# Performance work log

Measured on AMD Instinct MI355X. Metric: run time of the kernel, lower is better.

Reference implementation:

```python
import jax, jax.numpy as jnp
import numpy as np

B, N, DIN, DOUT = 16, 256, 64, 64
TEMP = 2.0          # temperatures[0]
POOL_K = 0.5        # pool_ratios[0]
BN_EPS = 1e-5


def setup_inputs() -> dict:
    key = jax.random.key(0)
    ks = jax.random.split(key, 8)
    g = lambda i, shape: (jax.random.normal(ks[i], shape, jnp.float32) * 0.08)
    return {
        "x": jax.random.normal(ks[0], (B, N, DIN), jnp.float32),
        # GraphAttentionLayer params
        "W_att": g(1, (DIN, DOUT)), "b_att": jnp.zeros((DOUT,), jnp.float32),
        "att_w": g(2, (DOUT,)),                      # att_weight [DOUT,1] squeezed
        "W_pwa": g(3, (DIN, DOUT)), "b_pwa": jnp.zeros((DOUT,), jnp.float32),
        "W_pna": g(4, (DIN, DOUT)), "b_pna": jnp.zeros((DOUT,), jnp.float32),
        "bn_scale": jnp.ones((DOUT,), jnp.float32),
        "bn_bias": jnp.zeros((DOUT,), jnp.float32),
        # GraphPool params
        "pool_w": g(5, (DOUT,)), "pool_b": jnp.zeros((), jnp.float32),
    }


def reference(x, W_att, b_att, att_w, W_pwa, b_pwa, W_pna, b_pna,
              bn_scale, bn_bias, pool_w, pool_b):
    # --- GraphAttentionLayer (eval mode: dropout = identity) ---
    # pairwise node multiplication: [B, i, j, DIN]
    pm = x[:, :, None, :] * x[:, None, :, :]
    att = jnp.tanh(jnp.einsum('bijd,de->bije', pm, W_att) + b_att)   # [B,N,N,DOUT]
    logits = jnp.einsum('bije,e->bij', att, att_w) / TEMP            # [B,N,N]
    # torch softmax over dim=-2 of [B,i,j,1] == axis j (the aggregated axis)
    A = jax.nn.softmax(logits, axis=2)                               # [B,N,N]
    agg = jnp.einsum('bij,bjd->bid', A, x)                           # [B,N,DIN]
    h = (agg @ W_pwa + b_pwa) + (x @ W_pna + b_pna)                  # [B,N,DOUT]
    # BatchNorm1d eval with running_mean=0, running_var=1
    h = h * (bn_scale / jnp.sqrt(1.0 + BN_EPS)) + bn_bias
    h = jax.nn.selu(h)
    # --- GraphPool (eval mode: dropout = identity) ---
    scores = jax.nn.sigmoid(h @ pool_w + pool_b)                     # [B,N]
    k = max(int(N * POOL_K), 1)
    _, idx = jax.lax.top_k(scores, k)                                # [B,k]
    hw = h * scores[:, :, None]
    out = jnp.take_along_axis(hw, idx[:, :, None], axis=1)           # [B,k,DOUT]
    return out
```

## Files before the change

kernel.cpp:

```cpp
#include <hip/hip_runtime.h>
#include <hip/hip_bf16.h>
#include <math.h>

#define BB 16
#define NN 256
#define DD 64
#define KTOP 128

typedef short s16x8 __attribute__((ext_vector_type(8)));
typedef float f32x4 __attribute__((ext_vector_type(4)));

typedef union { s16x8 v; unsigned u[4]; } frag_u;
typedef union { __hip_bfloat162 b2; unsigned u; } cvu;

__device__ __forceinline__ float asf(unsigned u){ union{unsigned u;float f;}c; c.u=u; return c.f; }

__device__ __forceinline__ void split2(float v0, float v1, unsigned& hu, unsigned& lu) {
    cvu c; c.b2 = __float22bfloat162_rn(make_float2(v0, v1));
    unsigned h = c.u;
    float l0 = v0 - asf(h << 16);
    float l1 = v1 - asf(h & 0xffff0000u);
    c.b2 = __float22bfloat162_rn(make_float2(l0, l1));
    hu = h; lu = c.u;
}

__global__ __launch_bounds__(512, 4) void k_fused(
    const float* __restrict__ x, const float* __restrict__ W_att,
    const float* __restrict__ b_att, const float* __restrict__ att_w,
    const float* __restrict__ Wpwa, const float* __restrict__ bpwa,
    const float* __restrict__ Wpna, const float* __restrict__ bpna,
    const float* __restrict__ bnsc, const float* __restrict__ bnbi,
    const float* __restrict__ poolw, const float* __restrict__ poolb,
    float* __restrict__ hbuf, float* __restrict__ scores)
{
    const int ig = blockIdx.x;
    const int b  = blockIdx.y;
    const int tid = threadIdx.x;
    const int w = tid >> 6, lane = tid & 63;
    const int quad = lane >> 4, c16 = lane & 15;
    const int jb = w * 32;
    const int ibase = ig * 4;

    __shared__ s16x8 sB[2][2][4][2][64];
    __shared__ float sXi[4 * 64];
    __shared__ float sL[4][256];
    __shared__ float sAgg[4][64];

    if (tid < 256) sXi[tid] = x[(b * NN + ibase + (tid >> 6)) * DD + (tid & 63)];

    const float L2E2 = 2.8853900817779268f;
    float bawL[4], aww[4];
    #pragma unroll
    for (int et = 0; et < 4; ++et) {
        bawL[et] = b_att[et * 16 + c16] * L2E2;
        aww[et]  = att_w[et * 16 + c16];
    }
    float halfS;
    {
        float sa = aww[0] + aww[1] + aww[2] + aww[3];
        sa += __shfl_xor(sa, 1); sa += __shfl_xor(sa, 2);
        sa += __shfl_xor(sa, 4); sa += __shfl_xor(sa, 8);
        halfS = 0.5f * sa;
    }

    const int bks = w >> 2, bet = w & 3;
    float wv[8];
    {
        const float* wp = &W_att[(bks * 32 + quad * 8) * 64 + bet * 16 + c16];
        #pragma unroll
        for (int t = 0; t < 8; ++t) wv[t] = wp[t * 64];
    }

    frag_u Ah[2][2], Al[2][2];
    #pragma unroll
    for (int jt = 0; jt < 2; ++jt) {
        #pragma unroll
        for (int ks = 0; ks < 2; ++ks) {
            const float* xr = &x[(b * NN + jb + jt * 16 + c16) * DD + ks * 32 + quad * 8];
            float4 a0 = *(const float4*)xr;
            float4 a1 = *(const float4*)(xr + 4);
            split2(a0.x, a0.y, Ah[jt][ks].u[0], Al[jt][ks].u[0]);
            split2(a0.z, a0.w, Ah[jt][ks].u[1], Al[jt][ks].u[1]);
            split2(a1.x, a1.y, Ah[jt][ks].u[2], Al[jt][ks].u[2]);
            split2(a1.z, a1.w, Ah[jt][ks].u[3], Al[jt][ks].u[3]);
        }
    }
    __syncthreads();

    {
        const float* xr = &sXi[0 * 64 + bks * 32 + quad * 8];
        float4 c0 = *(const float4*)xr;
        float4 c1 = *(const float4*)(xr + 4);
        float xiv[8] = {c0.x,c0.y,c0.z,c0.w,c1.x,c1.y,c1.z,c1.w};
        frag_u bh, bl;
        split2(wv[0] * xiv[0], wv[1] * xiv[1], bh.u[0], bl.u[0]);
        split2(wv[2] * xiv[2], wv[3] * xiv[3], bh.u[1], bl.u[1]);
        split2(wv[4] * xiv[4], wv[5] * xiv[5], bh.u[2], bl.u[2]);
        split2(wv[6] * xiv[6], wv[7] * xiv[7], bh.u[3], bl.u[3]);
        sB[0][bks][bet][0][lane] = bh.v;
        sB[0][bks][bet][1][lane] = bl.v;
    }

    #pragma unroll
    for (int ii = 0; ii < 4; ++ii) {
        __syncthreads();

        if (ii < 3) {
            const float* xr = &sXi[(ii + 1) * 64 + bks * 32 + quad * 8];
            float4 c0 = *(const float4*)xr;
            float4 c1 = *(const float4*)(xr + 4);
            float xiv[8] = {c0.x,c0.y,c0.z,c0.w,c1.x,c1.y,c1.z,c1.w};
            frag_u bh, bl;
            split2(wv[0] * xiv[0], wv[1] * xiv[1], bh.u[0], bl.u[0]);
            split2(wv[2] * xiv[2], wv[3] * xiv[3], bh.u[1], bl.u[1]);
            split2(wv[4] * xiv[4], wv[5] * xiv[5], bh.u[2], bl.u[2]);
            split2(wv[6] * xiv[6], wv[7] * xiv[7], bh.u[3], bl.u[3]);
            sB[(ii + 1) & 1][bks][bet][0][lane] = bh.v;
            sB[(ii + 1) & 1][bks][bet][1][lane] = bl.v;
        }

        const int cur = ii & 1;
        float p[2][4];
        #pragma unroll
        for (int jt = 0; jt < 2; ++jt)
            #pragma unroll
            for (int r = 0; r < 4; ++r) p[jt][r] = 0.0f;

        #pragma unroll
        for (int eth = 0; eth < 2; ++eth) {
            f32x4 acc[2][2];
            #pragma unroll
            for (int jt = 0; jt < 2; ++jt)
                #pragma unroll
                for (int e2 = 0; e2 < 2; ++e2)
                    acc[jt][e2] = (f32x4){0.f, 0.f, 0.f, 0.f};

            #pragma unroll
            for (int ks = 0; ks < 2; ++ks) {
                #pragma unroll
                for (int e2 = 0; e2 < 2; ++e2) {
                    const int et = eth * 2 + e2;
                    s16x8 bh = sB[cur][ks][et][0][lane];
                    s16x8 bl = sB[cur][ks][et][1][lane];
                    #pragma unroll
                    for (int jt = 0; jt < 2; ++jt) {
                        acc[jt][e2] = __builtin_amdgcn_mfma_f32_16x16x32_bf16(Ah[jt][ks].v, bh, acc[jt][e2], 0, 0, 0);
                        acc[jt][e2] = __builtin_amdgcn_mfma_f32_16x16x32_bf16(Al[jt][ks].v, bh, acc[jt][e2], 0, 0, 0);
                        acc[jt][e2] = __builtin_amdgcn_mfma_f32_16x16x32_bf16(Ah[jt][ks].v, bl, acc[jt][e2], 0, 0, 0);
                    }
                }
            }

            #pragma unroll
            for (int e2 = 0; e2 < 2; ++e2) {
                const int et = eth * 2 + e2;
                #pragma unroll
                for (int jt = 0; jt < 2; ++jt) {
                    #pragma unroll
                    for (int r = 0; r < 4; ++r) {
                        float arg = fmaf(acc[jt][e2][r], L2E2, bawL[et]);
                        float m = __builtin_amdgcn_exp2f(arg);
                        float rc = __builtin_amdgcn_rcpf(m + 1.0f);
                        p[jt][r] = fmaf(aww[et], rc, p[jt][r]);
                    }
                }
            }
        }

        #pragma unroll
        for (int jt = 0; jt < 2; ++jt) {
            #pragma unroll
            for (int r = 0; r < 4; ++r) {
                float s = p[jt][r];
                s += __shfl_xor(s, 1);
                s += __shfl_xor(s, 2);
                s += __shfl_xor(s, 4);
                s += __shfl_xor(s, 8);
                if (c16 == 0) sL[ii][jb + jt * 16 + quad * 4 + r] = halfS - s;
            }
        }
    }
    __syncthreads();

    if (w < 4) {
        const int i = ibase + w;
        float* row = sL[w];
        float lg0 = row[lane], lg1 = row[lane + 64], lg2 = row[lane + 128], lg3 = row[lane + 192];
        float m = fmaxf(fmaxf(lg0, lg1), fmaxf(lg2, lg3));
        #pragma unroll
        for (int off = 32; off; off >>= 1) m = fmaxf(m, __shfl_xor(m, off));
        float e0 = __expf(lg0 - m), e1 = __expf(lg1 - m), e2 = __expf(lg2 - m), e3 = __expf(lg3 - m);
        float ssum = e0 + e1 + e2 + e3;
        #pragma unroll
        for (int off = 32; off; off >>= 1) ssum += __shfl_xor(ssum, off);
        float inv = 1.0f / ssum;
        row[lane] = e0 * inv; row[lane + 64] = e1 * inv;
        row[lane + 128] = e2 * inv; row[lane + 192] = e3 * inv;
        __asm__ volatile("s_waitcnt lgkmcnt(0)" ::: "memory");

        float agg = 0.0f;
        const float4* A4 = (const float4*)row;
        const float* xb = &x[(b * NN) * DD];
        #pragma unroll 8
        for (int jq = 0; jq < 64; ++jq) {
            float4 a = A4[jq];
            int j = jq * 4;
            agg = fmaf(a.x, xb[(j + 0) * DD + lane], agg);
            agg = fmaf(a.y, xb[(j + 1) * DD + lane], agg);
            agg = fmaf(a.z, xb[(j + 2) * DD + lane], agg);
            agg = fmaf(a.w, xb[(j + 3) * DD + lane], agg);
        }
        sAgg[w][lane] = agg;
        __asm__ volatile("s_waitcnt lgkmcnt(0)" ::: "memory");

        double hacc = (double)bpwa[lane] + (double)bpna[lane];
        #pragma unroll 4
        for (int d = 0; d < 64; ++d) {
            hacc += (double)sAgg[w][d] * (double)Wpwa[d * DD + lane]
                  + (double)sXi[w * 64 + d] * (double)Wpna[d * DD + lane];
        }
        const double bnmul = 0.99999500003749968750e0;
        double hb = hacc * ((double)bnsc[lane] * bnmul) + (double)bnbi[lane];
        float hf = (float)hb;
        const float LAM = 1.0507009873554805f, ALP = 1.6732632423543772f;
        float hs = hf > 0.0f ? LAM * hf : LAM * ALP * (__expf(hf) - 1.0f);
        hbuf[((b * NN) + i) * DD + lane] = hs;

        double z = (double)hs * (double)poolw[lane];
        #pragma unroll
        for (int off = 32; off; off >>= 1) z += __shfl_xor(z, off);
        if (lane == 0) {
            double zz = z + (double)poolb[0];
            scores[b * NN + i] = (float)(1.0 / (1.0 + exp(-zz)));
        }
    }
}

__global__ __launch_bounds__(256) void k_topk(
    const float* __restrict__ scores, const float* __restrict__ hbuf,
    float* __restrict__ out)
{
    const int c = blockIdx.x;
    const int b = blockIdx.y;
    const int t = threadIdx.x;
    __shared__ float ss[256];
    __shared__ int   perm[16];
    ss[t] = scores[b * NN + t];
    __syncthreads();
    const float my = ss[t];
    int rank = 0;
    #pragma unroll 8
    for (int j = 0; j < 256; ++j) {
        float v = ss[j];
        rank += (v > my) || (v == my && j < t);
    }
    if ((rank >> 4) == c) perm[rank & 15] = t;
    __syncthreads();
    #pragma unroll
    for (int m = t; m < 16 * DD; m += 256) {
        int r = m >> 6, e = m & 63;
        int i = perm[r];
        out[(b * KTOP + c * 16 + r) * DD + e] = hbuf[((b * NN) + i) * DD + e] * ss[i];
    }
}

extern "C" void kernel_launch(void* const* d_in, const int* in_sizes, int n_in,
                              void* d_out, int out_size, void* d_ws, size_t ws_size,
                              hipStream_t stream) {
    const float* x        = (const float*)d_in[0];
    const float* W_att    = (const float*)d_in[1];
    const float* b_att    = (const float*)d_in[2];
    const float* att_w    = (const float*)d_in[3];
    const float* W_pwa    = (const float*)d_in[4];
    const float* b_pwa    = (const float*)d_in[5];
    const float* W_pna    = (const float*)d_in[6];
    const float* b_pna    = (const float*)d_in[7];
    const float* bn_scale = (const float*)d_in[8];
    const float* bn_bias  = (const float*)d_in[9];
    const float* pool_w   = (const float*)d_in[10];
    const float* pool_b   = (const float*)d_in[11];

    float* hbuf    = (float*)d_ws;
    float* scoresW = hbuf + BB * NN * DD;
    float* out     = (float*)d_out;

    k_fused<<<dim3(64, BB), 512, 0, stream>>>(x, W_att, b_att, att_w,
                                              W_pwa, b_pwa, W_pna, b_pna,
                                              bn_scale, bn_bias, pool_w, pool_b,
                                              hbuf, scoresW);
    k_topk<<<dim3(8, BB), 256, 0, stream>>>(scoresW, hbuf, out);
}
```

Before: 136.4 us.

## Transpose MFMA operands, seed accumulators with bias, raise occupancy target

Swaps the MFMA operand roles so the pairwise-weight tile is the A operand and x rows are B. Each lane's accumulator then holds the j-column sums, and the logit reduction needs only two cross-quad shuffles instead of four shuffles per element. Bias is loaded into the accumulator initial value, W_att is re-read from global instead of held in registers, and b_att/att_w move to shared memory, all to cut register use so launch bounds can target 6 waves per SIMD. The aggregation loop gets four independent accumulators to break the FMA dependency chain. Risks include extra global loads of W_att per iteration, register spills, and slight changes to summation order.

```diff
diff --git a/kernel.cpp b/kernel.cpp
--- a/kernel.cpp
+++ b/kernel.cpp
@@ -24,7 +24,7 @@
     hu = h; lu = c.u;
 }
 
-__global__ __launch_bounds__(512, 4) void k_fused(
+__global__ __launch_bounds__(512, 6) void k_fused(
     const float* __restrict__ x, const float* __restrict__ W_att,
     const float* __restrict__ b_att, const float* __restrict__ att_w,
     const float* __restrict__ Wpwa, const float* __restrict__ bpwa,
@@ -45,33 +45,31 @@
     __shared__ float sXi[4 * 64];
     __shared__ float sL[4][256];
     __shared__ float sAgg[4][64];
+    __shared__ float sBatt[64];
+    __shared__ float sAww[64];
 
     if (tid < 256) sXi[tid] = x[(b * NN + ibase + (tid >> 6)) * DD + (tid & 63)];
+    if (tid < 64) sBatt[tid] = b_att[tid];
+    else if (tid < 128) sAww[tid - 64] = att_w[tid - 64];
 
     const float L2E2 = 2.8853900817779268f;
-    float bawL[4], aww[4];
-    #pragma unroll
-    for (int et = 0; et < 4; ++et) {
-        bawL[et] = b_att[et * 16 + c16] * L2E2;
-        aww[et]  = att_w[et * 16 + c16];
-    }
+
     float halfS;
     {
-        float sa = aww[0] + aww[1] + aww[2] + aww[3];
-        sa += __shfl_xor(sa, 1); sa += __shfl_xor(sa, 2);
-        sa += __shfl_xor(sa, 4); sa += __shfl_xor(sa, 8);
+        float sa = 0.0f;
+        #pragma unroll
+        for (int mt = 0; mt < 4; ++mt) {
+            float4 a4 = ((const float4*)att_w)[mt * 4 + quad];
+            sa += (a4.x + a4.y) + (a4.z + a4.w);
+        }
+        sa += __shfl_xor(sa, 16);
+        sa += __shfl_xor(sa, 32);
         halfS = 0.5f * sa;
     }
 
-    const int bks = w >> 2, bet = w & 3;
-    float wv[8];
-    {
-        const float* wp = &W_att[(bks * 32 + quad * 8) * 64 + bet * 16 + c16];
-        #pragma unroll
-        for (int t = 0; t < 8; ++t) wv[t] = wp[t * 64];
-    }
-
-    frag_u Ah[2][2], Al[2][2];
+    const int bks = w >> 2, bmt = w & 3;
+
+    frag_u Xh[2][2], Xl[2][2];
     #pragma unroll
     for (int jt = 0; jt < 2; ++jt) {
         #pragma unroll
@@ -79,10 +77,10 @@
             const float* xr = &x[(b * NN + jb + jt * 16 + c16) * DD + ks * 32 + quad * 8];
             float4 a0 = *(const float4*)xr;
             float4 a1 = *(const float4*)(xr + 4);
-            split2(a0.x, a0.y, Ah[jt][ks].u[0], Al[jt][ks].u[0]);
-            split2(a0.z, a0.w, Ah[jt][ks].u[1], Al[jt][ks].u[1]);
-            split2(a1.x, a1.y, Ah[jt][ks].u[2], Al[jt][ks].u[2]);
-            split2(a1.z, a1.w, Ah[jt][ks].u[3], Al[jt][ks].u[3]);
+            split2(a0.x, a0.y, Xh[jt][ks].u[0], Xl[jt][ks].u[0]);
+            split2(a0.z, a0.w, Xh[jt][ks].u[1], Xl[jt][ks].u[1]);
+            split2(a1.x, a1.y, Xh[jt][ks].u[2], Xl[jt][ks].u[2]);
+            split2(a1.z, a1.w, Xh[jt][ks].u[3], Xl[jt][ks].u[3]);
         }
     }
     __syncthreads();
@@ -92,13 +90,14 @@
         float4 c0 = *(const float4*)xr;
         float4 c1 = *(const float4*)(xr + 4);
         float xiv[8] = {c0.x,c0.y,c0.z,c0.w,c1.x,c1.y,c1.z,c1.w};
+        const float* wp = &W_att[(bks * 32 + quad * 8) * 64 + bmt * 16 + c16];
         frag_u bh, bl;
-        split2(wv[0] * xiv[0], wv[1] * xiv[1], bh.u[0], bl.u[0]);
-        split2(wv[2] * xiv[2], wv[3] * xiv[3], bh.u[1], bl.u[1]);
-        split2(wv[4] * xiv[4], wv[5] * xiv[5], bh.u[2], bl.u[2]);
-        split2(wv[6] * xiv[6], wv[7] * xiv[7], bh.u[3], bl.u[3]);
-        sB[0][bks][bet][0][lane] = bh.v;
-        sB[0][bks][bet][1][lane] = bl.v;
+        split2(wp[0] * xiv[0], wp[64] * xiv[1], bh.u[0], bl.u[0]);
+        split2(wp[128] * xiv[2], wp[192] * xiv[3], bh.u[1], bl.u[1]);
+        split2(wp[256] * xiv[4], wp[320] * xiv[5], bh.u[2], bl.u[2]);
+        split2(wp[384] * xiv[6], wp[448] * xiv[7], bh.u[3], bl.u[3]);
+        sB[0][bks][bmt][0][lane] = bh.v;
+        sB[0][bks][bmt][1][lane] = bl.v;
     }
 
     #pragma unroll
@@ -110,74 +109,74 @@
             float4 c0 = *(const float4*)xr;
             float4 c1 = *(const float4*)(xr + 4);
             float xiv[8] = {c0.x,c0.y,c0.z,c0.w,c1.x,c1.y,c1.z,c1.w};
+            const float* wp = &W_att[(bks * 32 + quad * 8) * 64 + bmt * 16 + c16];
             frag_u bh, bl;
-            split2(wv[0] * xiv[0], wv[1] * xiv[1], bh.u[0], bl.u[0]);
-            split2(wv[2] * xiv[2], wv[3] * xiv[3], bh.u[1], bl.u[1]);
-            split2(wv[4] * xiv[4], wv[5] * xiv[5], bh.u[2], bl.u[2]);
-            split2(wv[6] * xiv[6], wv[7] * xiv[7], bh.u[3], bl.u[3]);
-            sB[(ii + 1) & 1][bks][bet][0][lane] = bh.v;
-            sB[(ii + 1) & 1][bks][bet][1][lane] = bl.v;
+            split2(wp[0] * xiv[0], wp[64] * xiv[1], bh.u[0], bl.u[0]);
+            split2(wp[128] * xiv[2], wp[192] * xiv[3], bh.u[1], bl.u[1]);
+            split2(wp[256] * xiv[4], wp[320] * xiv[5], bh.u[2], bl.u[2]);
+            split2(wp[384] * xiv[6], wp[448] * xiv[7], bh.u[3], bl.u[3]);
+            sB[(ii + 1) & 1][bks][bmt][0][lane] = bh.v;
+            sB[(ii + 1) & 1][bks][bmt][1][lane] = bl.v;
         }
 
         const int cur = ii & 1;
-        float p[2][4];
-        #pragma unroll
-        for (int jt = 0; jt < 2; ++jt)
-            #pragma unroll
-            for (int r = 0; r < 4; ++r) p[jt][r] = 0.0f;
+        float s0 = 0.0f, s1 = 0.0f;
 
         #pragma unroll
         for (int eth = 0; eth < 2; ++eth) {
             f32x4 acc[2][2];
             #pragma unroll
-            for (int jt = 0; jt < 2; ++jt)
-                #pragma unroll
-                for (int e2 = 0; e2 < 2; ++e2)
-                    acc[jt][e2] = (f32x4){0.f, 0.f, 0.f, 0.f};
+            for (int e2 = 0; e2 < 2; ++e2) {
+                f32x4 bi = *(const f32x4*)&sBatt[(eth * 2 + e2) * 16 + quad * 4];
+                acc[e2][0] = bi;
+                acc[e2][1] = bi;
+            }
 
             #pragma unroll
             for (int ks = 0; ks < 2; ++ks) {
                 #pragma unroll
                 for (int e2 = 0; e2 < 2; ++e2) {
-                    const int et = eth * 2 + e2;
-                    s16x8 bh = sB[cur][ks][et][0][lane];
-                    s16x8 bl = sB[cur][ks][et][1][lane];
+                    const int mt = eth * 2 + e2;
+                    s16x8 ah = sB[cur][ks][mt][0][lane];
+                    s16x8 al = sB[cur][ks][mt][1][lane];
                     #pragma unroll
                     for (int jt = 0; jt < 2; ++jt) {
-                        acc[jt][e2] = __builtin_amdgcn_mfma_f32_16x16x32_bf16(Ah[jt][ks].v, bh, acc[jt][e2], 0, 0, 0);
-                        acc[jt][e2] = __builtin_amdgcn_mfma_f32_16x16x32_bf16(Al[jt][ks].v, bh, acc[jt][e2], 0, 0, 0);
-                        acc[jt][e2] = __builtin_amdgcn_mfma_f32_16x16x32_bf16(Ah[jt][ks].v, bl, acc[jt][e2], 0, 0, 0);
+                        acc[e2][jt] = __builtin_amdgcn_mfma_f32_16x16x32_bf16(ah, Xh[jt][ks].v, acc[e2][jt], 0, 0, 0);
+                        acc[e2][jt] = __builtin_amdgcn_mfma_f32_16x16x32_bf16(al, Xh[jt][ks].v, acc[e2][jt], 0, 0, 0);
+                        acc[e2][jt] = __builtin_amdgcn_mfma_f32_16x16x32_bf16(ah, Xl[jt][ks].v, acc[e2][jt], 0, 0, 0);
                     }
                 }
             }
 
             #pragma unroll
             for (int e2 = 0; e2 < 2; ++e2) {
-                const int et = eth * 2 + e2;
+                const int mt = eth * 2 + e2;
+                f32x4 awwv = *(const f32x4*)&sAww[mt * 16 + quad * 4];
                 #pragma unroll
-                for (int jt = 0; jt < 2; ++jt) {
-                    #pragma unroll
-                    for (int r = 0; r < 4; ++r) {
-                        float arg = fmaf(acc[jt][e2][r], L2E2, bawL[et]);
+                for (int r = 0; r < 4; ++r) {
+                    {
+                        float arg = acc[e2][0][r] * L2E2;
                         float m = __builtin_amdgcn_exp2f(arg);
                         float rc = __builtin_amdgcn_rcpf(m + 1.0f);
-                        p[jt][r] = fmaf(aww[et], rc, p[jt][r]);
+                        s0 = fmaf(awwv[r], rc, s0);
+                    }
+                    {
+                        float arg = acc[e2][1][r] * L2E2;
+                        float m = __builtin_amdgcn_exp2f(arg);
+                        float rc = __builtin_amdgcn_rcpf(m + 1.0f);
+                        s1 = fmaf(awwv[r], rc, s1);
                     }
                 }
             }
         }
 
-        #pragma unroll
-        for (int jt = 0; jt < 2; ++jt) {
-            #pragma unroll
-            for (int r = 0; r < 4; ++r) {
-                float s = p[jt][r];
-                s += __shfl_xor(s, 1);
-                s += __shfl_xor(s, 2);
-                s += __shfl_xor(s, 4);
-                s += __shfl_xor(s, 8);
-                if (c16 == 0) sL[ii][jb + jt * 16 + quad * 4 + r] = halfS - s;
-            }
+        s0 += __shfl_xor(s0, 16);
+        s0 += __shfl_xor(s0, 32);
+        s1 += __shfl_xor(s1, 16);
+        s1 += __shfl_xor(s1, 32);
+        if (quad == 0) {
+            sL[ii][jb + c16]      = halfS - s0;
+            sL[ii][jb + 16 + c16] = halfS - s1;
         }
     }
     __syncthreads();
@@ -198,19 +197,19 @@
         row[lane + 128] = e2 * inv; row[lane + 192] = e3 * inv;
         __asm__ volatile("s_waitcnt lgkmcnt(0)" ::: "memory");
 
-        float agg = 0.0f;
+        float ag0 = 0.f, ag1 = 0.f, ag2 = 0.f, ag3 = 0.f;
         const float4* A4 = (const float4*)row;
         const float* xb = &x[(b * NN) * DD];
         #pragma unroll 8
         for (int jq = 0; jq < 64; ++jq) {
             float4 a = A4[jq];
             int j = jq * 4;
-            agg = fmaf(a.x, xb[(j + 0) * DD + lane], agg);
-            agg = fmaf(a.y, xb[(j + 1) * DD + lane], agg);
-            agg = fmaf(a.z, xb[(j + 2) * DD + lane], agg);
-            agg = fmaf(a.w, xb[(j + 3) * DD + lane], agg);
-        }
-        sAgg[w][lane] = agg;
+            ag0 = fmaf(a.x, xb[(j + 0) * DD + lane], ag0);
+            ag1 = fmaf(a.y, xb[(j + 1) * DD + lane], ag1);
+            ag2 = fmaf(a.z, xb[(j + 2) * DD + lane], ag2);
+            ag3 = fmaf(a.w, xb[(j + 3) * DD + lane], ag3);
+        }
+        sAgg[w][lane] = (ag0 + ag1) + (ag2 + ag3);
         __asm__ volatile("s_waitcnt lgkmcnt(0)" ::: "memory");
 
         double hacc = (double)bpwa[lane] + (double)bpna[lane];
```

Measured after the change: 139.6 us. 2.4% more time.
